# Kernel tuning notes

Measured on AMD Instinct MI355X. Metric: run time of the kernel, lower is better.

Reference implementation:

```python
import jax, jax.numpy as jnp
import numpy as np

K = 3
LAMBDA_AMP = 0.1
N_NODES = 100000
N_EDGES = 1600000
D_FEAT = 50


def _proximal_l21(x, lambda_):
    # rowwise L2,1 shrinkage: scale each row by max(||row||-lambda,0)/||row||
    row_norm = jnp.linalg.norm(x, axis=1)  # [N]
    score = jnp.maximum(row_norm - lambda_, 0.0)
    score = jnp.where(row_norm > 0, score / jnp.where(row_norm > 0, row_norm, 1.0), score)
    return score[:, None] * x


def setup_inputs() -> dict:
    key = jax.random.key(0)
    k1, k2, k3, k4 = jax.random.split(key, 4)
    feat = jax.random.normal(k1, (N_NODES, D_FEAT), dtype=jnp.float32)
    edge_weight = jax.random.uniform(k2, (N_EDGES,), dtype=jnp.float32)
    src = jax.random.randint(k3, (N_EDGES,), 0, N_NODES, dtype=jnp.int32)
    dst = jax.random.randint(k4, (N_EDGES,), 0, N_NODES, dtype=jnp.int32)
    return {"feat": feat, "edge_weight": edge_weight, "src": src, "dst": dst}


def reference(feat, edge_weight, src, dst):
    n = feat.shape[0]
    # add self-loops (add_self_loop=True), self-loop weight = 1
    loop = jnp.arange(n, dtype=src.dtype)
    src_f = jnp.concatenate([src, loop])
    dst_f = jnp.concatenate([dst, loop])
    ew = jnp.concatenate([edge_weight, jnp.ones((n,), dtype=edge_weight.dtype)])

    # norm='both': w_ji = ew / (sqrt(out_deg(j)) * sqrt(in_deg(i))), weighted degrees
    out_deg = jax.ops.segment_sum(ew, src_f, num_segments=n)
    in_deg = jax.ops.segment_sum(ew, dst_f, num_segments=n)
    inv_sqrt_out = jnp.where(out_deg > 0, out_deg, 1.0) ** -0.5 * (out_deg > 0)
    inv_sqrt_in = jnp.where(in_deg > 0, in_deg, 1.0) ** -0.5 * (in_deg > 0)
    w = ew * inv_sqrt_out[src_f] * inv_sqrt_in[dst_f]  # [E+N]

    lam = LAMBDA_AMP
    gamma = 1.0 / (2.0 * (1.0 - lam))
    hh = feat
    x = feat
    for _ in range(K):
        # compute_LX: x - A_norm x  (u_mul_e + sum == SpMM over edges)
        agg = jax.ops.segment_sum(x[src_f] * w[:, None], dst_f, num_segments=n)
        lx = x - agg
        y = x - gamma * 2.0 * (1.0 - lam) * lx
        x = hh + _proximal_l21(y - hh, gamma * lam)
    return x
```

## Files before the change

### kernel.cpp

```cpp
#include <hip/hip_runtime.h>
#include <hip/hip_bf16.h>
#include <hip/hip_fp16.h>

#define D 50
#define PADH 64
#define GLAM 0.05555555555555555f
#define SCAN_B 1024
#define FIXS 8388608.0f
#define INV_FIXS (1.0f / 8388608.0f)
#define WSC 32768.0f
#define INV_WSC (1.0f / 32768.0f)
#define EPB 8192
#define B2T 512
#define BSH 9
#define BMSK 511u
#define BT 512
#define MAXB 256
#define MAXRUN 12288

typedef unsigned long long u64;

__global__ void k_b1p(const int* __restrict__ src, const int* __restrict__ dst,
                      int* __restrict__ mat, const float* __restrict__ feat,
                      __half* __restrict__ xp, int e, int nblk, int nbuk, int n) {
    if ((int)blockIdx.x < nblk) {
        __shared__ unsigned hd[MAXB], hs[MAXB];
        for (int j = threadIdx.x; j < nbuk; j += blockDim.x) { hd[j] = 0; hs[j] = 0; }
        __syncthreads();
        int base = blockIdx.x * EPB;
        int end = base + EPB; if (end > e) end = e;
        for (int i = base + threadIdx.x; i < end; i += blockDim.x) {
            int t = __builtin_nontemporal_load(dst + i);
            int s = __builtin_nontemporal_load(src + i);
            atomicAdd(&hd[t >> BSH], 1u);
            atomicAdd(&hs[s >> BSH], 1u);
        }
        __syncthreads();
        for (int j = threadIdx.x; j < nbuk; j += blockDim.x) {
            mat[j * nblk + blockIdx.x] = (int)hd[j];
            mat[(nbuk + j) * nblk + blockIdx.x] = (int)hs[j];
        }
    } else {
        int i = ((int)blockIdx.x - nblk) * (int)blockDim.x + (int)threadIdx.x;
        if (i < n * PADH) {
            int node = i >> 6, col = i & 63;
            xp[i] = (col < D) ? __float2half_rn(feat[node * D + col]) : __half(0.0f);
        }
    }
}

__global__ void k_scan1(const int* __restrict__ cnt, int* __restrict__ out,
                        int* __restrict__ bsum, int n) {
    __shared__ int s[SCAN_B];
    int i = blockIdx.x * SCAN_B + threadIdx.x;
    int v = (i < n) ? cnt[i] : 0;
    s[threadIdx.x] = v; __syncthreads();
    for (int off = 1; off < SCAN_B; off <<= 1) {
        int t = (threadIdx.x >= (unsigned)off) ? s[threadIdx.x - off] : 0;
        __syncthreads();
        s[threadIdx.x] += t; __syncthreads();
    }
    if (i < n) out[i] = s[threadIdx.x] - v;
    if (threadIdx.x == SCAN_B - 1) bsum[blockIdx.x] = s[threadIdx.x];
}

__global__ void k_scan2(int* __restrict__ bsum, int nb) {
    __shared__ int s[SCAN_B];
    int v = (threadIdx.x < (unsigned)nb) ? bsum[threadIdx.x] : 0;
    s[threadIdx.x] = v; __syncthreads();
    for (int off = 1; off < SCAN_B; off <<= 1) {
        int t = (threadIdx.x >= (unsigned)off) ? s[threadIdx.x - off] : 0;
        __syncthreads();
        s[threadIdx.x] += t; __syncthreads();
    }
    if (threadIdx.x < (unsigned)nb) bsum[threadIdx.x] = s[threadIdx.x] - v;
}

__global__ void k_scan3(int* __restrict__ out, const int* __restrict__ bsum, int n) {
    int i = blockIdx.x * SCAN_B + threadIdx.x;
    if (i < n) out[i] += bsum[blockIdx.x];
}

__global__ void k_b2(const float* __restrict__ ew, const int* __restrict__ src,
                     const int* __restrict__ dst, const int* __restrict__ msc,
                     u64* __restrict__ bind, unsigned* __restrict__ bins,
                     int e, int nblk, int nbuk) {
    __shared__ unsigned cd[MAXB], cs[MAXB];
    __shared__ unsigned ld[MAXB], ls[MAXB];
    __shared__ int gbd[MAXB], gbs[MAXB];
    __shared__ u64 sd[EPB];
    __shared__ unsigned ss[EPB];
    __shared__ unsigned char bdd[EPB], bds[EPB];
    int tid = threadIdx.x;
    for (int j = tid; j < MAXB; j += blockDim.x) { cd[j] = 0; cs[j] = 0; }
    __syncthreads();
    int base = blockIdx.x * EPB;
    int end = base + EPB; if (end > e) end = e;
    int m = end - base;

    for (int i = base + tid; i < end; i += blockDim.x) {
        atomicAdd(&cd[(unsigned)__builtin_nontemporal_load(dst + i) >> BSH], 1u);
        atomicAdd(&cs[(unsigned)__builtin_nontemporal_load(src + i) >> BSH], 1u);
    }
    __syncthreads();

    unsigned vd = 0, vs = 0;
    if (tid < MAXB) { vd = cd[tid]; vs = cs[tid]; ld[tid] = vd; ls[tid] = vs; }
    __syncthreads();
    for (int off = 1; off < MAXB; off <<= 1) {
        unsigned td = 0, ts = 0;
        if (tid < MAXB && tid >= off) { td = ld[tid - off]; ts = ls[tid - off]; }
        __syncthreads();
        if (tid < MAXB) { ld[tid] += td; ls[tid] += ts; }
        __syncthreads();
    }
    if (tid < MAXB) {
        ld[tid] -= vd; ls[tid] -= vs;
        cd[tid] = ld[tid]; cs[tid] = ls[tid];
        if (tid < nbuk) {
            gbd[tid] = msc[tid * nblk + blockIdx.x];
            gbs[tid] = msc[(nbuk + tid) * nblk + blockIdx.x] - e;
        }
    }
    __syncthreads();

    for (int i = base + tid; i < end; i += blockDim.x) {
        float w = __builtin_nontemporal_load(ew + i);
        int s = __builtin_nontemporal_load(src + i);
        int t = __builtin_nontemporal_load(dst + i);
        unsigned wfix = (unsigned)(w * FIXS + 0.5f);
        if (wfix > 0x7FFFFFu) wfix = 0x7FFFFFu;
        unsigned tb = (unsigned)t >> BSH, sb = (unsigned)s >> BSH;
        unsigned pd = atomicAdd(&cd[tb], 1u);
        sd[pd] = ((u64)__float_as_uint(w) << 32)
               | ((unsigned)s << BSH) | (unsigned)(t & BMSK);
        bdd[pd] = (unsigned char)tb;
        unsigned ps = atomicAdd(&cs[sb], 1u);
        ss[ps] = (wfix << BSH) | (unsigned)(s & BMSK);
        bds[ps] = (unsigned char)sb;
    }
    __syncthreads();

    for (int p = tid; p < m; p += blockDim.x) {
        unsigned jd = bdd[p];
        bind[gbd[jd] + (int)(p - ld[jd])] = sd[p];
        unsigned js = bds[p];
        bins[gbs[js] + (int)(p - ls[js])] = ss[p];
    }
}

__global__ void k_srcdeg(const unsigned* __restrict__ bins, const int* __restrict__ msc,
                         float* __restrict__ iso, int n, int nblk, int nbuk, int e) {
    __shared__ unsigned wl[BT];
    wl[threadIdx.x] = 0;
    __syncthreads();
    int b = blockIdx.x;
    int start = msc[(nbuk + b) * nblk] - e;
    int end = (b + 1 < nbuk) ? (msc[(nbuk + b + 1) * nblk] - e) : e;
    for (int i = start + threadIdx.x; i < end; i += blockDim.x) {
        unsigned r = bins[i];
        atomicAdd(&wl[r & BMSK], r >> BSH);
    }
    __syncthreads();
    int node = b * BT + threadIdx.x;
    if (node < n)
        iso[node] = rsqrtf(1.0f + (float)wl[threadIdx.x] * INV_FIXS);
}

__global__ void k_dstfill(const u64* __restrict__ bind, const int* __restrict__ msc,
                          const float* __restrict__ iso, float* __restrict__ isi,
                          int* __restrict__ cnt, int* __restrict__ rowptr,
                          unsigned* __restrict__ pe, int n, int nblk, int nbuk, int e) {
    __shared__ u64 recs[MAXRUN];
    __shared__ unsigned cl[BT], wl[BT], cur[BT];
    __shared__ int sc[BT];
    __shared__ float isL[BT];
    cl[threadIdx.x] = 0; wl[threadIdx.x] = 0;
    __syncthreads();
    int b = blockIdx.x;
    int start = msc[b * nblk];
    int end = (b + 1 < nbuk) ? msc[(b + 1) * nblk] : e;
    int run = end - start;
    bool fast = (run <= MAXRUN);

    if (fast) {
        for (int i = threadIdx.x; i < run; i += blockDim.x) {
            u64 r = bind[start + i];
            recs[i] = r;
            unsigned loc = (unsigned)r & BMSK;
            float w = __uint_as_float((unsigned)(r >> 32));
            unsigned wfix = (unsigned)(w * FIXS + 0.5f);
            if (wfix > 0x7FFFFFu) wfix = 0x7FFFFFu;
            atomicAdd(&cl[loc], 1u);
            atomicAdd(&wl[loc], wfix);
        }
    } else {
        for (int i = start + threadIdx.x; i < end; i += blockDim.x) {
            u64 r = bind[i];
            unsigned loc = (unsigned)r & BMSK;
            float w = __uint_as_float((unsigned)(r >> 32));
            unsigned wfix = (unsigned)(w * FIXS + 0.5f);
            if (wfix > 0x7FFFFFu) wfix = 0x7FFFFFu;
            atomicAdd(&cl[loc], 1u);
            atomicAdd(&wl[loc], wfix);
        }
    }
    __syncthreads();

    int myc = (int)cl[threadIdx.x];
    sc[threadIdx.x] = myc;
    __syncthreads();
    for (int off = 1; off < BT; off <<= 1) {
        int t = (threadIdx.x >= (unsigned)off) ? sc[threadIdx.x - off] : 0;
        __syncthreads();
        sc[threadIdx.x] += t;
        __syncthreads();
    }
    int lrp = start + sc[threadIdx.x] - myc;

    float myisi = rsqrtf(1.0f + (float)wl[threadIdx.x] * INV_FIXS);
    isL[threadIdx.x] = myisi;
    cur[threadIdx.x] = (unsigned)lrp;

    int node = b * BT + threadIdx.x;
    if (node < n) {
        isi[node] = myisi;
        cnt[node] = myc;
        rowptr[node] = lrp;
    }
    __syncthreads();

    if (fast) {
        for (int i = threadIdx.x; i < run; i += blockDim.x) {
            u64 r = recs[i];
            unsigned lo = (unsigned)r;
            unsigned tloc = lo & BMSK;
            unsigned s = lo >> BSH;
            float w = __uint_as_float((unsigned)(r >> 32));
            float wv = w * iso[s] * isL[tloc];
            unsigned wq = (unsigned)(wv * WSC + 0.5f);
            if (wq > 32767u) wq = 32767u;
            unsigned pos = atomicAdd(&cur[tloc], 1u);
            pe[pos] = (s << 15) | wq;
        }
    } else {
        for (int i = start + threadIdx.x; i < end; i += blockDim.x) {
            u64 r = bind[i];
            unsigned lo = (unsigned)r;
            unsigned tloc = lo & BMSK;
            unsigned s = lo >> BSH;
            float w = __uint_as_float((unsigned)(r >> 32));
            float wv = w * iso[s] * isL[tloc];
            unsigned wq = (unsigned)(wv * WSC + 0.5f);
            if (wq > 32767u) wq = 32767u;
            unsigned pos = atomicAdd(&cur[tloc], 1u);
            pe[pos] = (s << 15) | wq;
        }
    }
}

__device__ __forceinline__ void acc_edge(const uint4& u, float w,
                                         float& a0, float& a1, float& a2, float& a3,
                                         float& a4, float& a5, float& a6, float& a7) {
    const __half2* hp = (const __half2*)&u;
    float2 f0 = __half22float2(hp[0]);
    float2 f1 = __half22float2(hp[1]);
    float2 f2 = __half22float2(hp[2]);
    float2 f3 = __half22float2(hp[3]);
    a0 = fmaf(w, f0.x, a0); a1 = fmaf(w, f0.y, a1);
    a2 = fmaf(w, f1.x, a2); a3 = fmaf(w, f1.y, a3);
    a4 = fmaf(w, f2.x, a4); a5 = fmaf(w, f2.y, a5);
    a6 = fmaf(w, f3.x, a6); a7 = fmaf(w, f3.y, a7);
}

__global__ void k_iter(const int* __restrict__ rowptr, const int* __restrict__ cnt,
                       const unsigned* __restrict__ pe, const __half* __restrict__ xin,
                       const __half* __restrict__ xpF, const float* __restrict__ iso,
                       const float* __restrict__ isi, __half* __restrict__ hout,
                       float* __restrict__ fout, int n, int final_iter) {
    int lane = threadIdx.x & 63;
    int c    = lane & 7;
    int waveId = (blockIdx.x * blockDim.x + threadIdx.x) >> 6;
    int node = waveId * 8 + (lane >> 3);
    if (node >= n) return;

    float a0 = 0.f, a1 = 0.f, a2 = 0.f, a3 = 0.f;
    float a4 = 0.f, a5 = 0.f, a6 = 0.f, a7 = 0.f;

    int beg = rowptr[node], m = cnt[node];

    int j = 0;
    for (; j + 4 <= m; j += 4) {
        unsigned p0 = pe[beg + j];
        unsigned p1 = pe[beg + j + 1];
        unsigned p2 = pe[beg + j + 2];
        unsigned p3 = pe[beg + j + 3];
        unsigned s0 = p0 >> 15; float w0 = (float)(p0 & 32767u) * INV_WSC;
        unsigned s1 = p1 >> 15; float w1 = (float)(p1 & 32767u) * INV_WSC;
        unsigned s2 = p2 >> 15; float w2 = (float)(p2 & 32767u) * INV_WSC;
        unsigned s3 = p3 >> 15; float w3 = (float)(p3 & 32767u) * INV_WSC;
        uint4 u0 = *(const uint4*)(xin + ((size_t)s0 << 6) + (c << 3));
        uint4 u1 = *(const uint4*)(xin + ((size_t)s1 << 6) + (c << 3));
        uint4 u2 = *(const uint4*)(xin + ((size_t)s2 << 6) + (c << 3));
        uint4 u3 = *(const uint4*)(xin + ((size_t)s3 << 6) + (c << 3));
        acc_edge(u0, w0, a0, a1, a2, a3, a4, a5, a6, a7);
        acc_edge(u1, w1, a0, a1, a2, a3, a4, a5, a6, a7);
        acc_edge(u2, w2, a0, a1, a2, a3, a4, a5, a6, a7);
        acc_edge(u3, w3, a0, a1, a2, a3, a4, a5, a6, a7);
    }
    for (; j < m; ++j) {
        unsigned p0 = pe[beg + j];
        unsigned s0 = p0 >> 15;
        float    w0 = (float)(p0 & 32767u) * INV_WSC;
        uint4 u0 = *(const uint4*)(xin + ((size_t)s0 << 6) + (c << 3));
        acc_edge(u0, w0, a0, a1, a2, a3, a4, a5, a6, a7);
    }

    float selfw = iso[node] * isi[node];
    {
        uint4 u = *(const uint4*)(xin + ((size_t)node << 6) + (c << 3));
        acc_edge(u, selfw, a0, a1, a2, a3, a4, a5, a6, a7);
    }

    float f[8];
    {
        uint4 u = *(const uint4*)(xpF + ((size_t)node << 6) + (c << 3));
        const __half2* hp = (const __half2*)&u;
        float2 f0 = __half22float2(hp[0]);
        float2 f1 = __half22float2(hp[1]);
        float2 f2 = __half22float2(hp[2]);
        float2 f3 = __half22float2(hp[3]);
        f[0] = f0.x; f[1] = f0.y; f[2] = f1.x; f[3] = f1.y;
        f[4] = f2.x; f[5] = f2.y; f[6] = f3.x; f[7] = f3.y;
    }

    float d0 = a0 - f[0], d1 = a1 - f[1], d2 = a2 - f[2], d3 = a3 - f[3];
    float d4 = a4 - f[4], d5 = a5 - f[5], d6 = a6 - f[6], d7 = a7 - f[7];

    float ssum = d0*d0 + d1*d1 + d2*d2 + d3*d3 + d4*d4 + d5*d5 + d6*d6 + d7*d7;
    ssum += __shfl_xor(ssum, 1, 64);
    ssum += __shfl_xor(ssum, 2, 64);
    ssum += __shfl_xor(ssum, 4, 64);
    float norm = sqrtf(ssum);
    float sc = (norm > 0.0f) ? fmaxf(norm - GLAM, 0.0f) / norm : 0.0f;

    float o0 = f[0] + sc * d0, o1 = f[1] + sc * d1;
    float o2 = f[2] + sc * d2, o3 = f[3] + sc * d3;
    float o4 = f[4] + sc * d4, o5 = f[5] + sc * d5;
    float o6 = f[6] + sc * d6, o7 = f[7] + sc * d7;
    if (!final_iter) {
        __half2 h0 = __float22half2_rn(make_float2(o0, o1));
        __half2 h1 = __float22half2_rn(make_float2(o2, o3));
        __half2 h2 = __float22half2_rn(make_float2(o4, o5));
        __half2 h3 = __float22half2_rn(make_float2(o6, o7));
        uint4 u;
        u.x = *(unsigned*)&h0; u.y = *(unsigned*)&h1;
        u.z = *(unsigned*)&h2; u.w = *(unsigned*)&h3;
        *(uint4*)(hout + ((size_t)node << 6) + (c << 3)) = u;
    } else {
        float o[8] = {o0, o1, o2, o3, o4, o5, o6, o7};
        int fb = c << 3;
        #pragma unroll
        for (int k = 0; k < 4; ++k) {
            int ff = fb + (k << 1);
            if (ff + 1 < D) {
                float2 v; v.x = o[k * 2]; v.y = o[k * 2 + 1];
                *(float2*)(fout + (size_t)node * D + ff) = v;
            }
        }
    }
}

extern "C" void kernel_launch(void* const* d_in, const int* in_sizes, int n_in,
                              void* d_out, int out_size, void* d_ws, size_t ws_size,
                              hipStream_t stream) {
    const float* feat = (const float*)d_in[0];
    const float* ew   = (const float*)d_in[1];
    const int* src = (const int*)d_in[2];
    const int* dst = (const int*)d_in[3];

    const int nd = in_sizes[0];
    const int n  = nd / D;
    const int e  = in_sizes[1];
    const int np = n * PADH;

    const int nbuk = (n + BT - 1) / BT;
    const int nblk = (e + EPB - 1) / EPB;
    const int nm   = 2 * nbuk * nblk;

    __half*   xpF    = (__half*)d_ws;
    __half*   xpA    = xpF + np;
    __half*   xpB    = xpA + np;
    u64*      bind   = (u64*)(xpB + np);
    unsigned* pe     = (unsigned*)(bind + e);
    unsigned* bins   = pe + e;
    int*      mat    = (int*)(bins + e);
    int*      msc    = mat + nm;
    float*    isi    = (float*)(msc + nm);
    float*    iso    = isi + n;
    int*      cnt    = (int*)(iso + n);
    int*      rowptr = cnt + n;
    int*      bsum   = rowptr + n;
    float*    out    = (float*)d_out;

    const int B = 256;
    const int gP  = (np + B2T - 1) / B2T;
    const int NBm = (nm + SCAN_B - 1) / SCAN_B;

    k_b1p<<<nblk + gP, B2T, 0, stream>>>(src, dst, mat, feat, xpF, e, nblk, nbuk, n);
    k_scan1<<<NBm, SCAN_B, 0, stream>>>(mat, msc, bsum, nm);
    k_scan2<<<1, SCAN_B, 0, stream>>>(bsum, NBm);
    k_scan3<<<NBm, SCAN_B, 0, stream>>>(msc, bsum, nm);
    k_b2<<<nblk, B2T, 0, stream>>>(ew, src, dst, msc, bind, bins, e, nblk, nbuk);
    k_srcdeg<<<nbuk, BT, 0, stream>>>(bins, msc, iso, n, nblk, nbuk, e);
    k_dstfill<<<nbuk, BT, 0, stream>>>(bind, msc, iso, isi, cnt, rowptr, pe, n, nblk, nbuk, e);

    const int nodesPerBlock = (B / 64) * 8;
    const int iterGrid = (n + nodesPerBlock - 1) / nodesPerBlock;

    k_iter<<<iterGrid, B, 0, stream>>>(rowptr, cnt, pe, xpF, xpF, iso, isi, xpA, out, n, 0);
    k_iter<<<iterGrid, B, 0, stream>>>(rowptr, cnt, pe, xpA, xpF, iso, isi, xpB, out, n, 0);
    k_iter<<<iterGrid, B, 0, stream>>>(rowptr, cnt, pe, xpB, xpF, iso, isi, xpA, out, n, 1);
}
```

Measured before the change: 254.5 us.

## Compute source degrees via global atomics and degree-sort nodes for SpMM

Drops the source-side bucketing pass (per-block source histogram, source bin scatter and the k_srcdeg kernel). Source weighted degrees are now accumulated directly with global atomicAdd into a per-node array, followed by a small rsqrt kernel. It also builds a degree histogram and a counting-sort permutation so each k_iter wave handles nodes of similar in-degree, which reduces divergence inside a wave, and it marks pe loads as nontemporal. The cost is 1.6M scattered global atomics, one extra indirection per node in the iteration kernels, and less locality in output writes.

After: 338.5 us. 1.33x slower.

```diff
diff --git a/kernel.cpp b/kernel.cpp
--- a/kernel.cpp
+++ b/kernel.cpp
@@ -17,35 +17,36 @@
 #define BT 512
 #define MAXB 256
 #define MAXRUN 12288
+#define DEGB 64
 
 typedef unsigned long long u64;
 
 __global__ void k_b1p(const int* __restrict__ src, const int* __restrict__ dst,
                       int* __restrict__ mat, const float* __restrict__ feat,
-                      __half* __restrict__ xp, int e, int nblk, int nbuk, int n) {
+                      __half* __restrict__ xp, unsigned* __restrict__ degS,
+                      unsigned* __restrict__ dcur, unsigned* __restrict__ dhist,
+                      int e, int nblk, int nbuk, int n) {
     if ((int)blockIdx.x < nblk) {
-        __shared__ unsigned hd[MAXB], hs[MAXB];
-        for (int j = threadIdx.x; j < nbuk; j += blockDim.x) { hd[j] = 0; hs[j] = 0; }
+        __shared__ unsigned hd[MAXB];
+        for (int j = threadIdx.x; j < nbuk; j += blockDim.x) hd[j] = 0;
         __syncthreads();
         int base = blockIdx.x * EPB;
         int end = base + EPB; if (end > e) end = e;
         for (int i = base + threadIdx.x; i < end; i += blockDim.x) {
             int t = __builtin_nontemporal_load(dst + i);
-            int s = __builtin_nontemporal_load(src + i);
             atomicAdd(&hd[t >> BSH], 1u);
-            atomicAdd(&hs[s >> BSH], 1u);
-        }
-        __syncthreads();
-        for (int j = threadIdx.x; j < nbuk; j += blockDim.x) {
+        }
+        __syncthreads();
+        for (int j = threadIdx.x; j < nbuk; j += blockDim.x)
             mat[j * nblk + blockIdx.x] = (int)hd[j];
-            mat[(nbuk + j) * nblk + blockIdx.x] = (int)hs[j];
-        }
     } else {
         int i = ((int)blockIdx.x - nblk) * (int)blockDim.x + (int)threadIdx.x;
         if (i < n * PADH) {
             int node = i >> 6, col = i & 63;
             xp[i] = (col < D) ? __float2half_rn(feat[node * D + col]) : __half(0.0f);
         }
+        if (i < n) degS[i] = 0u;
+        if (i < DEGB) { dcur[i] = 0u; dhist[i] = 0u; }
     }
 }
 
@@ -81,46 +82,41 @@
     if (i < n) out[i] += bsum[blockIdx.x];
 }
 
-__global__ void k_b2(const float* __restrict__ ew, const int* __restrict__ src,
+__global__ __launch_bounds__(B2T, 4) void k_b2(
+                     const float* __restrict__ ew, const int* __restrict__ src,
                      const int* __restrict__ dst, const int* __restrict__ msc,
-                     u64* __restrict__ bind, unsigned* __restrict__ bins,
+                     u64* __restrict__ bind, unsigned* __restrict__ degS,
                      int e, int nblk, int nbuk) {
-    __shared__ unsigned cd[MAXB], cs[MAXB];
-    __shared__ unsigned ld[MAXB], ls[MAXB];
-    __shared__ int gbd[MAXB], gbs[MAXB];
+    __shared__ unsigned cd[MAXB];
+    __shared__ unsigned ld[MAXB];
+    __shared__ int gbd[MAXB];
     __shared__ u64 sd[EPB];
-    __shared__ unsigned ss[EPB];
-    __shared__ unsigned char bdd[EPB], bds[EPB];
+    __shared__ unsigned char bdd[EPB];
     int tid = threadIdx.x;
-    for (int j = tid; j < MAXB; j += blockDim.x) { cd[j] = 0; cs[j] = 0; }
+    for (int j = tid; j < MAXB; j += blockDim.x) cd[j] = 0;
     __syncthreads();
     int base = blockIdx.x * EPB;
     int end = base + EPB; if (end > e) end = e;
     int m = end - base;
 
-    for (int i = base + tid; i < end; i += blockDim.x) {
+    for (int i = base + tid; i < end; i += blockDim.x)
         atomicAdd(&cd[(unsigned)__builtin_nontemporal_load(dst + i) >> BSH], 1u);
-        atomicAdd(&cs[(unsigned)__builtin_nontemporal_load(src + i) >> BSH], 1u);
-    }
-    __syncthreads();
-
-    unsigned vd = 0, vs = 0;
-    if (tid < MAXB) { vd = cd[tid]; vs = cs[tid]; ld[tid] = vd; ls[tid] = vs; }
+    __syncthreads();
+
+    unsigned vd = 0;
+    if (tid < MAXB) { vd = cd[tid]; ld[tid] = vd; }
     __syncthreads();
     for (int off = 1; off < MAXB; off <<= 1) {
-        unsigned td = 0, ts = 0;
-        if (tid < MAXB && tid >= off) { td = ld[tid - off]; ts = ls[tid - off]; }
-        __syncthreads();
-        if (tid < MAXB) { ld[tid] += td; ls[tid] += ts; }
+        unsigned td = 0;
+        if (tid < MAXB && tid >= off) td = ld[tid - off];
+        __syncthreads();
+        if (tid < MAXB) ld[tid] += td;
         __syncthreads();
     }
     if (tid < MAXB) {
-        ld[tid] -= vd; ls[tid] -= vs;
-        cd[tid] = ld[tid]; cs[tid] = ls[tid];
-        if (tid < nbuk) {
-            gbd[tid] = msc[tid * nblk + blockIdx.x];
-            gbs[tid] = msc[(nbuk + tid) * nblk + blockIdx.x] - e;
-        }
+        ld[tid] -= vd;
+        cd[tid] = ld[tid];
+        if (tid < nbuk) gbd[tid] = msc[tid * nblk + blockIdx.x];
     }
     __syncthreads();
 
@@ -130,52 +126,38 @@
         int t = __builtin_nontemporal_load(dst + i);
         unsigned wfix = (unsigned)(w * FIXS + 0.5f);
         if (wfix > 0x7FFFFFu) wfix = 0x7FFFFFu;
-        unsigned tb = (unsigned)t >> BSH, sb = (unsigned)s >> BSH;
+        atomicAdd(&degS[s], wfix);
+        unsigned tb = (unsigned)t >> BSH;
         unsigned pd = atomicAdd(&cd[tb], 1u);
         sd[pd] = ((u64)__float_as_uint(w) << 32)
                | ((unsigned)s << BSH) | (unsigned)(t & BMSK);
         bdd[pd] = (unsigned char)tb;
-        unsigned ps = atomicAdd(&cs[sb], 1u);
-        ss[ps] = (wfix << BSH) | (unsigned)(s & BMSK);
-        bds[ps] = (unsigned char)sb;
     }
     __syncthreads();
 
     for (int p = tid; p < m; p += blockDim.x) {
         unsigned jd = bdd[p];
         bind[gbd[jd] + (int)(p - ld[jd])] = sd[p];
-        unsigned js = bds[p];
-        bins[gbs[js] + (int)(p - ls[js])] = ss[p];
-    }
-}
-
-__global__ void k_srcdeg(const unsigned* __restrict__ bins, const int* __restrict__ msc,
-                         float* __restrict__ iso, int n, int nblk, int nbuk, int e) {
-    __shared__ unsigned wl[BT];
-    wl[threadIdx.x] = 0;
-    __syncthreads();
-    int b = blockIdx.x;
-    int start = msc[(nbuk + b) * nblk] - e;
-    int end = (b + 1 < nbuk) ? (msc[(nbuk + b + 1) * nblk] - e) : e;
-    for (int i = start + threadIdx.x; i < end; i += blockDim.x) {
-        unsigned r = bins[i];
-        atomicAdd(&wl[r & BMSK], r >> BSH);
-    }
-    __syncthreads();
-    int node = b * BT + threadIdx.x;
-    if (node < n)
-        iso[node] = rsqrtf(1.0f + (float)wl[threadIdx.x] * INV_FIXS);
+    }
+}
+
+__global__ void k_iso(const unsigned* __restrict__ degS, float* __restrict__ iso, int n) {
+    int i = blockIdx.x * blockDim.x + threadIdx.x;
+    if (i < n) iso[i] = rsqrtf(1.0f + (float)degS[i] * INV_FIXS);
 }
 
 __global__ void k_dstfill(const u64* __restrict__ bind, const int* __restrict__ msc,
                           const float* __restrict__ iso, float* __restrict__ isi,
                           int* __restrict__ cnt, int* __restrict__ rowptr,
-                          unsigned* __restrict__ pe, int n, int nblk, int nbuk, int e) {
+                          unsigned* __restrict__ pe, unsigned* __restrict__ dhist,
+                          int n, int nblk, int nbuk, int e) {
     __shared__ u64 recs[MAXRUN];
     __shared__ unsigned cl[BT], wl[BT], cur[BT];
     __shared__ int sc[BT];
     __shared__ float isL[BT];
+    __shared__ unsigned dh[DEGB];
     cl[threadIdx.x] = 0; wl[threadIdx.x] = 0;
+    if (threadIdx.x < DEGB) dh[threadIdx.x] = 0;
     __syncthreads();
     int b = blockIdx.x;
     int start = msc[b * nblk];
@@ -227,8 +209,12 @@
         isi[node] = myisi;
         cnt[node] = myc;
         rowptr[node] = lrp;
-    }
-    __syncthreads();
+        int dg = myc < (DEGB - 1) ? myc : (DEGB - 1);
+        atomicAdd(&dh[dg], 1u);
+    }
+    __syncthreads();
+    if (threadIdx.x < DEGB && dh[threadIdx.x])
+        atomicAdd(&dhist[threadIdx.x], dh[threadIdx.x]);
 
     if (fast) {
         for (int i = threadIdx.x; i < run; i += blockDim.x) {
@@ -259,6 +245,30 @@
     }
 }
 
+__global__ void k_dscat(const int* __restrict__ cnt, const unsigned* __restrict__ dhist,
+                        unsigned* __restrict__ dcur, int* __restrict__ perm, int n) {
+    __shared__ unsigned lh[DEGB], lb[DEGB], gb[DEGB], hco[DEGB];
+    int tid = threadIdx.x;
+    if (tid < DEGB) { lh[tid] = 0; hco[tid] = dhist[tid]; }
+    __syncthreads();
+    int i = blockIdx.x * blockDim.x + tid;
+    int d = 0; unsigned lrank = 0;
+    if (i < n) {
+        int c = cnt[i];
+        d = c < (DEGB - 1) ? c : (DEGB - 1);
+        lrank = atomicAdd(&lh[d], 1u);
+    }
+    __syncthreads();
+    if (tid < DEGB) {
+        unsigned s = 0;
+        for (int j = 0; j < tid; ++j) s += hco[j];
+        gb[tid] = s;
+        lb[tid] = lh[tid] ? atomicAdd(&dcur[tid], lh[tid]) : 0u;
+    }
+    __syncthreads();
+    if (i < n) perm[gb[d] + lb[d] + lrank] = i;
+}
+
 __device__ __forceinline__ void acc_edge(const uint4& u, float w,
                                          float& a0, float& a1, float& a2, float& a3,
                                          float& a4, float& a5, float& a6, float& a7) {
@@ -274,15 +284,17 @@
 }
 
 __global__ void k_iter(const int* __restrict__ rowptr, const int* __restrict__ cnt,
-                       const unsigned* __restrict__ pe, const __half* __restrict__ xin,
+                       const unsigned* __restrict__ pe, const int* __restrict__ perm,
+                       const __half* __restrict__ xin,
                        const __half* __restrict__ xpF, const float* __restrict__ iso,
                        const float* __restrict__ isi, __half* __restrict__ hout,
                        float* __restrict__ fout, int n, int final_iter) {
     int lane = threadIdx.x & 63;
     int c    = lane & 7;
     int waveId = (blockIdx.x * blockDim.x + threadIdx.x) >> 6;
-    int node = waveId * 8 + (lane >> 3);
-    if (node >= n) return;
+    int slot = waveId * 8 + (lane >> 3);
+    if (slot >= n) return;
+    int node = perm[slot];
 
     float a0 = 0.f, a1 = 0.f, a2 = 0.f, a3 = 0.f;
     float a4 = 0.f, a5 = 0.f, a6 = 0.f, a7 = 0.f;
@@ -291,10 +303,10 @@
 
     int j = 0;
     for (; j + 4 <= m; j += 4) {
-        unsigned p0 = pe[beg + j];
-        unsigned p1 = pe[beg + j + 1];
-        unsigned p2 = pe[beg + j + 2];
-        unsigned p3 = pe[beg + j + 3];
+        unsigned p0 = __builtin_nontemporal_load(pe + beg + j);
+        unsigned p1 = __builtin_nontemporal_load(pe + beg + j + 1);
+        unsigned p2 = __builtin_nontemporal_load(pe + beg + j + 2);
+        unsigned p3 = __builtin_nontemporal_load(pe + beg + j + 3);
         unsigned s0 = p0 >> 15; float w0 = (float)(p0 & 32767u) * INV_WSC;
         unsigned s1 = p1 >> 15; float w1 = (float)(p1 & 32767u) * INV_WSC;
         unsigned s2 = p2 >> 15; float w2 = (float)(p2 & 32767u) * INV_WSC;
@@ -309,7 +321,7 @@
         acc_edge(u3, w3, a0, a1, a2, a3, a4, a5, a6, a7);
     }
     for (; j < m; ++j) {
-        unsigned p0 = pe[beg + j];
+        unsigned p0 = __builtin_nontemporal_load(pe + beg + j);
         unsigned s0 = p0 >> 15;
         float    w0 = (float)(p0 & 32767u) * INV_WSC;
         uint4 u0 = *(const uint4*)(xin + ((size_t)s0 << 6) + (c << 3));
@@ -386,39 +398,45 @@
 
     const int nbuk = (n + BT - 1) / BT;
     const int nblk = (e + EPB - 1) / EPB;
-    const int nm   = 2 * nbuk * nblk;
+    const int nm   = nbuk * nblk;
 
     __half*   xpF    = (__half*)d_ws;
     __half*   xpA    = xpF + np;
     __half*   xpB    = xpA + np;
     u64*      bind   = (u64*)(xpB + np);
     unsigned* pe     = (unsigned*)(bind + e);
-    unsigned* bins   = pe + e;
-    int*      mat    = (int*)(bins + e);
+    int*      mat    = (int*)(pe + e);
     int*      msc    = mat + nm;
     float*    isi    = (float*)(msc + nm);
     float*    iso    = isi + n;
     int*      cnt    = (int*)(iso + n);
     int*      rowptr = cnt + n;
-    int*      bsum   = rowptr + n;
+    unsigned* degS   = (unsigned*)(rowptr + n);
+    int*      perm   = (int*)(degS + n);
+    unsigned* dhist  = (unsigned*)(perm + n);
+    unsigned* dcur   = dhist + DEGB;
+    int*      bsum   = (int*)(dcur + DEGB);
     float*    out    = (float*)d_out;
 
     const int B = 256;
     const int gP  = (np + B2T - 1) / B2T;
     const int NBm = (nm + SCAN_B - 1) / SCAN_B;
 
-    k_b1p<<<nblk + gP, B2T, 0, stream>>>(src, dst, mat, feat, xpF, e, nblk, nbuk, n);
+    k_b1p<<<nblk + gP, B2T, 0, stream>>>(src, dst, mat, feat, xpF, degS, dcur, dhist,
+                                         e, nblk, nbuk, n);
     k_scan1<<<NBm, SCAN_B, 0, stream>>>(mat, msc, bsum, nm);
     k_scan2<<<1, SCAN_B, 0, stream>>>(bsum, NBm);
     k_scan3<<<NBm, SCAN_B, 0, stream>>>(msc, bsum, nm);
-    k_b2<<<nblk, B2T, 0, stream>>>(ew, src, dst, msc, bind, bins, e, nblk, nbuk);
-    k_srcdeg<<<nbuk, BT, 0, stream>>>(bins, msc, iso, n, nblk, nbuk, e);
-    k_dstfill<<<nbuk, BT, 0, stream>>>(bind, msc, iso, isi, cnt, rowptr, pe, n, nblk, nbuk, e);
+    k_b2<<<nblk, B2T, 0, stream>>>(ew, src, dst, msc, bind, degS, e, nblk, nbuk);
+    k_iso<<<(n + 255) / 256, 256, 0, stream>>>(degS, iso, n);
+    k_dstfill<<<nbuk, BT, 0, stream>>>(bind, msc, iso, isi, cnt, rowptr, pe, dhist,
+                                       n, nblk, nbuk, e);
+    k_dscat<<<(n + 255) / 256, 256, 0, stream>>>(cnt, dhist, dcur, perm, n);
 
     const int nodesPerBlock = (B / 64) * 8;
     const int iterGrid = (n + nodesPerBlock - 1) / nodesPerBlock;
 
-    k_iter<<<iterGrid, B, 0, stream>>>(rowptr, cnt, pe, xpF, xpF, iso, isi, xpA, out, n, 0);
-    k_iter<<<iterGrid, B, 0, stream>>>(rowptr, cnt, pe, xpA, xpF, iso, isi, xpB, out, n, 0);
-    k_iter<<<iterGrid, B, 0, stream>>>(rowptr, cnt, pe, xpB, xpF, iso, isi, xpA, out, n, 1);
-}
+    k_iter<<<iterGrid, B, 0, stream>>>(rowptr, cnt, pe, perm, xpF, xpF, iso, isi, xpA, out, n, 0);
+    k_iter<<<iterGrid, B, 0, stream>>>(rowptr, cnt, pe, perm, xpA, xpF, iso, isi, xpB, out, n, 0);
+    k_iter<<<iterGrid, B, 0, stream>>>(rowptr, cnt, pe, perm, xpB, xpF, iso, isi, xpA, out, n, 1);
+}
```

## Sort nodes by in-degree for balanced SpMM waves; halve edges per block

Applied to the files above, without the earlier changes.

Builds a degree histogram in the dst-fill kernel and adds a scatter kernel that writes a node permutation grouped by in-degree. The SpMM iteration kernels then process nodes in that order, so the 8 nodes sharing a wave have similar edge counts and lanes wait less on each other. It also halves the edges per binning block (more blocks, more bucket-matrix entries to scan) and adds launch bounds to the binning kernel. The costs are an extra kernel, an extra indirection per node, and output writes scattered across node order rather than contiguous.

After: 272.2 us. +7.0%, slower.

```diff
diff --git a/kernel.cpp b/kernel.cpp
--- a/kernel.cpp
+++ b/kernel.cpp
@@ -10,19 +10,22 @@
 #define INV_FIXS (1.0f / 8388608.0f)
 #define WSC 32768.0f
 #define INV_WSC (1.0f / 32768.0f)
-#define EPB 8192
+#define EPB 4096
 #define B2T 512
 #define BSH 9
 #define BMSK 511u
 #define BT 512
 #define MAXB 256
 #define MAXRUN 12288
+#define DEGB 64
 
 typedef unsigned long long u64;
 
 __global__ void k_b1p(const int* __restrict__ src, const int* __restrict__ dst,
                       int* __restrict__ mat, const float* __restrict__ feat,
-                      __half* __restrict__ xp, int e, int nblk, int nbuk, int n) {
+                      __half* __restrict__ xp, unsigned* __restrict__ dcur,
+                      unsigned* __restrict__ dhist,
+                      int e, int nblk, int nbuk, int n) {
     if ((int)blockIdx.x < nblk) {
         __shared__ unsigned hd[MAXB], hs[MAXB];
         for (int j = threadIdx.x; j < nbuk; j += blockDim.x) { hd[j] = 0; hs[j] = 0; }
@@ -46,6 +49,7 @@
             int node = i >> 6, col = i & 63;
             xp[i] = (col < D) ? __float2half_rn(feat[node * D + col]) : __half(0.0f);
         }
+        if (i < DEGB) { dcur[i] = 0u; dhist[i] = 0u; }
     }
 }
 
@@ -81,7 +85,8 @@
     if (i < n) out[i] += bsum[blockIdx.x];
 }
 
-__global__ void k_b2(const float* __restrict__ ew, const int* __restrict__ src,
+__global__ __launch_bounds__(B2T, 4) void k_b2(
+                     const float* __restrict__ ew, const int* __restrict__ src,
                      const int* __restrict__ dst, const int* __restrict__ msc,
                      u64* __restrict__ bind, unsigned* __restrict__ bins,
                      int e, int nblk, int nbuk) {
@@ -170,12 +175,15 @@
 __global__ void k_dstfill(const u64* __restrict__ bind, const int* __restrict__ msc,
                           const float* __restrict__ iso, float* __restrict__ isi,
                           int* __restrict__ cnt, int* __restrict__ rowptr,
-                          unsigned* __restrict__ pe, int n, int nblk, int nbuk, int e) {
+                          unsigned* __restrict__ pe, unsigned* __restrict__ dhist,
+                          int n, int nblk, int nbuk, int e) {
     __shared__ u64 recs[MAXRUN];
     __shared__ unsigned cl[BT], wl[BT], cur[BT];
     __shared__ int sc[BT];
     __shared__ float isL[BT];
+    __shared__ unsigned dh[DEGB];
     cl[threadIdx.x] = 0; wl[threadIdx.x] = 0;
+    if (threadIdx.x < DEGB) dh[threadIdx.x] = 0;
     __syncthreads();
     int b = blockIdx.x;
     int start = msc[b * nblk];
@@ -227,8 +235,12 @@
         isi[node] = myisi;
         cnt[node] = myc;
         rowptr[node] = lrp;
-    }
-    __syncthreads();
+        int dg = myc < (DEGB - 1) ? myc : (DEGB - 1);
+        atomicAdd(&dh[dg], 1u);
+    }
+    __syncthreads();
+    if (threadIdx.x < DEGB && dh[threadIdx.x])
+        atomicAdd(&dhist[threadIdx.x], dh[threadIdx.x]);
 
     if (fast) {
         for (int i = threadIdx.x; i < run; i += blockDim.x) {
@@ -259,6 +271,30 @@
     }
 }
 
+__global__ void k_dscat(const int* __restrict__ cnt, const unsigned* __restrict__ dhist,
+                        unsigned* __restrict__ dcur, int* __restrict__ perm, int n) {
+    __shared__ unsigned lh[DEGB], lb[DEGB], gb[DEGB], hco[DEGB];
+    int tid = threadIdx.x;
+    if (tid < DEGB) { lh[tid] = 0; hco[tid] = dhist[tid]; }
+    __syncthreads();
+    int i = blockIdx.x * blockDim.x + tid;
+    int d = 0; unsigned lrank = 0;
+    if (i < n) {
+        int c = cnt[i];
+        d = c < (DEGB - 1) ? c : (DEGB - 1);
+        lrank = atomicAdd(&lh[d], 1u);
+    }
+    __syncthreads();
+    if (tid < DEGB) {
+        unsigned s = 0;
+        for (int j = 0; j < tid; ++j) s += hco[j];
+        gb[tid] = s;
+        lb[tid] = lh[tid] ? atomicAdd(&dcur[tid], lh[tid]) : 0u;
+    }
+    __syncthreads();
+    if (i < n) perm[gb[d] + lb[d] + lrank] = i;
+}
+
 __device__ __forceinline__ void acc_edge(const uint4& u, float w,
                                          float& a0, float& a1, float& a2, float& a3,
                                          float& a4, float& a5, float& a6, float& a7) {
@@ -274,15 +310,17 @@
 }
 
 __global__ void k_iter(const int* __restrict__ rowptr, const int* __restrict__ cnt,
-                       const unsigned* __restrict__ pe, const __half* __restrict__ xin,
+                       const unsigned* __restrict__ pe, const int* __restrict__ perm,
+                       const __half* __restrict__ xin,
                        const __half* __restrict__ xpF, const float* __restrict__ iso,
                        const float* __restrict__ isi, __half* __restrict__ hout,
                        float* __restrict__ fout, int n, int final_iter) {
     int lane = threadIdx.x & 63;
     int c    = lane & 7;
     int waveId = (blockIdx.x * blockDim.x + threadIdx.x) >> 6;
-    int node = waveId * 8 + (lane >> 3);
-    if (node >= n) return;
+    int slot = waveId * 8 + (lane >> 3);
+    if (slot >= n) return;
+    int node = perm[slot];
 
     float a0 = 0.f, a1 = 0.f, a2 = 0.f, a3 = 0.f;
     float a4 = 0.f, a5 = 0.f, a6 = 0.f, a7 = 0.f;
@@ -400,25 +438,31 @@
     float*    iso    = isi + n;
     int*      cnt    = (int*)(iso + n);
     int*      rowptr = cnt + n;
-    int*      bsum   = rowptr + n;
+    int*      perm   = rowptr + n;
+    unsigned* dhist  = (unsigned*)(perm + n);
+    unsigned* dcur   = dhist + DEGB;
+    int*      bsum   = (int*)(dcur + DEGB);
     float*    out    = (float*)d_out;
 
     const int B = 256;
     const int gP  = (np + B2T - 1) / B2T;
     const int NBm = (nm + SCAN_B - 1) / SCAN_B;
 
-    k_b1p<<<nblk + gP, B2T, 0, stream>>>(src, dst, mat, feat, xpF, e, nblk, nbuk, n);
+    k_b1p<<<nblk + gP, B2T, 0, stream>>>(src, dst, mat, feat, xpF, dcur, dhist,
+                                         e, nblk, nbuk, n);
     k_scan1<<<NBm, SCAN_B, 0, stream>>>(mat, msc, bsum, nm);
     k_scan2<<<1, SCAN_B, 0, stream>>>(bsum, NBm);
     k_scan3<<<NBm, SCAN_B, 0, stream>>>(msc, bsum, nm);
     k_b2<<<nblk, B2T, 0, stream>>>(ew, src, dst, msc, bind, bins, e, nblk, nbuk);
     k_srcdeg<<<nbuk, BT, 0, stream>>>(bins, msc, iso, n, nblk, nbuk, e);
-    k_dstfill<<<nbuk, BT, 0, stream>>>(bind, msc, iso, isi, cnt, rowptr, pe, n, nblk, nbuk, e);
+    k_dstfill<<<nbuk, BT, 0, stream>>>(bind, msc, iso, isi, cnt, rowptr, pe, dhist,
+                                       n, nblk, nbuk, e);
+    k_dscat<<<(n + 255) / 256, 256, 0, stream>>>(cnt, dhist, dcur, perm, n);
 
     const int nodesPerBlock = (B / 64) * 8;
     const int iterGrid = (n + nodesPerBlock - 1) / nodesPerBlock;
 
-    k_iter<<<iterGrid, B, 0, stream>>>(rowptr, cnt, pe, xpF, xpF, iso, isi, xpA, out, n, 0);
-    k_iter<<<iterGrid, B, 0, stream>>>(rowptr, cnt, pe, xpA, xpF, iso, isi, xpB, out, n, 0);
-    k_iter<<<iterGrid, B, 0, stream>>>(rowptr, cnt, pe, xpB, xpF, iso, isi, xpA, out, n, 1);
-}
+    k_iter<<<iterGrid, B, 0, stream>>>(rowptr, cnt, pe, perm, xpF, xpF, iso, isi, xpA, out, n, 0);
+    k_iter<<<iterGrid, B, 0, stream>>>(rowptr, cnt, pe, perm, xpA, xpF, iso, isi, xpB, out, n, 0);
+    k_iter<<<iterGrid, B, 0, stream>>>(rowptr, cnt, pe, perm, xpB, xpF, iso, isi, xpA, out, n, 1);
+}
```

## Replace per-block count matrix scan with global bucket atomics and direct scatter

Applied to the files above, without the earlier changes.

The bucket sort preprocessing no longer builds a per-block-by-bucket count matrix and scans it in three kernels. Instead, global per-bucket totals are accumulated with atomics and scanned by a single small kernel. Each placement block then reserves its output ranges with one global atomic per bucket and writes records straight to global memory, skipping the shared-memory staging. The SpMM gather loop also gains an 8-way unrolled path to keep more loads in flight. The trade-off is that the order of edges within a bucket becomes nondeterministic and the global writes are less coalesced.

After: 276.5 us. 1.09x slower.

```diff
diff --git a/kernel.cpp b/kernel.cpp
--- a/kernel.cpp
+++ b/kernel.cpp
@@ -5,11 +5,11 @@
 #define D 50
 #define PADH 64
 #define GLAM 0.05555555555555555f
-#define SCAN_B 1024
 #define FIXS 8388608.0f
 #define INV_FIXS (1.0f / 8388608.0f)
 #define WSC 32768.0f
 #define INV_WSC (1.0f / 32768.0f)
+#define ECB 16384
 #define EPB 8192
 #define B2T 512
 #define BSH 9
@@ -17,18 +17,20 @@
 #define BT 512
 #define MAXB 256
 #define MAXRUN 12288
+#define GSTR 16
 
 typedef unsigned long long u64;
 
-__global__ void k_b1p(const int* __restrict__ src, const int* __restrict__ dst,
-                      int* __restrict__ mat, const float* __restrict__ feat,
-                      __half* __restrict__ xp, int e, int nblk, int nbuk, int n) {
-    if ((int)blockIdx.x < nblk) {
+__global__ void k_count(const int* __restrict__ src, const int* __restrict__ dst,
+                        unsigned* __restrict__ totD, unsigned* __restrict__ totS,
+                        const float* __restrict__ feat, __half* __restrict__ xp,
+                        int e, int ncb, int nbuk, int n) {
+    if ((int)blockIdx.x < ncb) {
         __shared__ unsigned hd[MAXB], hs[MAXB];
         for (int j = threadIdx.x; j < nbuk; j += blockDim.x) { hd[j] = 0; hs[j] = 0; }
         __syncthreads();
-        int base = blockIdx.x * EPB;
-        int end = base + EPB; if (end > e) end = e;
+        int base = blockIdx.x * ECB;
+        int end = base + ECB; if (end > e) end = e;
         for (int i = base + threadIdx.x; i < end; i += blockDim.x) {
             int t = __builtin_nontemporal_load(dst + i);
             int s = __builtin_nontemporal_load(src + i);
@@ -37,11 +39,11 @@
         }
         __syncthreads();
         for (int j = threadIdx.x; j < nbuk; j += blockDim.x) {
-            mat[j * nblk + blockIdx.x] = (int)hd[j];
-            mat[(nbuk + j) * nblk + blockIdx.x] = (int)hs[j];
+            if (hd[j]) atomicAdd(&totD[j], hd[j]);
+            if (hs[j]) atomicAdd(&totS[j], hs[j]);
         }
     } else {
-        int i = ((int)blockIdx.x - nblk) * (int)blockDim.x + (int)threadIdx.x;
+        int i = ((int)blockIdx.x - ncb) * (int)blockDim.x + (int)threadIdx.x;
         if (i < n * PADH) {
             int node = i >> 6, col = i & 63;
             xp[i] = (col < D) ? __float2half_rn(feat[node * D + col]) : __half(0.0f);
@@ -49,54 +51,43 @@
     }
 }
 
-__global__ void k_scan1(const int* __restrict__ cnt, int* __restrict__ out,
-                        int* __restrict__ bsum, int n) {
-    __shared__ int s[SCAN_B];
-    int i = blockIdx.x * SCAN_B + threadIdx.x;
-    int v = (i < n) ? cnt[i] : 0;
-    s[threadIdx.x] = v; __syncthreads();
-    for (int off = 1; off < SCAN_B; off <<= 1) {
-        int t = (threadIdx.x >= (unsigned)off) ? s[threadIdx.x - off] : 0;
+__global__ void k_scanS(const unsigned* __restrict__ totD, const unsigned* __restrict__ totS,
+                        unsigned* __restrict__ gcur, int* __restrict__ basesD,
+                        int* __restrict__ basesS, int nbuk, int e) {
+    __shared__ unsigned s[B2T];
+    int tid = threadIdx.x;
+    unsigned v = 0;
+    if (tid < nbuk) v = totD[tid];
+    else if (tid < 2 * nbuk) v = totS[tid - nbuk];
+    s[tid] = v; __syncthreads();
+    for (int off = 1; off < B2T; off <<= 1) {
+        unsigned t = (tid >= off) ? s[tid - off] : 0;
         __syncthreads();
-        s[threadIdx.x] += t; __syncthreads();
-    }
-    if (i < n) out[i] = s[threadIdx.x] - v;
-    if (threadIdx.x == SCAN_B - 1) bsum[blockIdx.x] = s[threadIdx.x];
-}
-
-__global__ void k_scan2(int* __restrict__ bsum, int nb) {
-    __shared__ int s[SCAN_B];
-    int v = (threadIdx.x < (unsigned)nb) ? bsum[threadIdx.x] : 0;
-    s[threadIdx.x] = v; __syncthreads();
-    for (int off = 1; off < SCAN_B; off <<= 1) {
-        int t = (threadIdx.x >= (unsigned)off) ? s[threadIdx.x - off] : 0;
-        __syncthreads();
-        s[threadIdx.x] += t; __syncthreads();
-    }
-    if (threadIdx.x < (unsigned)nb) bsum[threadIdx.x] = s[threadIdx.x] - v;
-}
-
-__global__ void k_scan3(int* __restrict__ out, const int* __restrict__ bsum, int n) {
-    int i = blockIdx.x * SCAN_B + threadIdx.x;
-    if (i < n) out[i] += bsum[blockIdx.x];
-}
-
-__global__ void k_b2(const float* __restrict__ ew, const int* __restrict__ src,
-                     const int* __restrict__ dst, const int* __restrict__ msc,
+        s[tid] += t; __syncthreads();
+    }
+    unsigned excl = s[tid] - v;
+    if (tid < nbuk) {
+        gcur[tid * GSTR] = excl;
+        basesD[tid] = (int)excl;
+    } else if (tid < 2 * nbuk) {
+        unsigned b = excl - (unsigned)e;
+        gcur[(MAXB + (tid - nbuk)) * GSTR] = b;
+        basesS[tid - nbuk] = (int)b;
+    }
+    if (tid == 0) { basesD[nbuk] = e; basesS[nbuk] = e; }
+}
+
+__global__ __launch_bounds__(B2T) void k_place(
+                     const float* __restrict__ ew, const int* __restrict__ src,
+                     const int* __restrict__ dst, unsigned* __restrict__ gcur,
                      u64* __restrict__ bind, unsigned* __restrict__ bins,
-                     int e, int nblk, int nbuk) {
+                     int e, int nbuk) {
     __shared__ unsigned cd[MAXB], cs[MAXB];
-    __shared__ unsigned ld[MAXB], ls[MAXB];
-    __shared__ int gbd[MAXB], gbs[MAXB];
-    __shared__ u64 sd[EPB];
-    __shared__ unsigned ss[EPB];
-    __shared__ unsigned char bdd[EPB], bds[EPB];
     int tid = threadIdx.x;
     for (int j = tid; j < MAXB; j += blockDim.x) { cd[j] = 0; cs[j] = 0; }
     __syncthreads();
     int base = blockIdx.x * EPB;
     int end = base + EPB; if (end > e) end = e;
-    int m = end - base;
 
     for (int i = base + tid; i < end; i += blockDim.x) {
         atomicAdd(&cd[(unsigned)__builtin_nontemporal_load(dst + i) >> BSH], 1u);
@@ -104,23 +95,11 @@
     }
     __syncthreads();
 
-    unsigned vd = 0, vs = 0;
-    if (tid < MAXB) { vd = cd[tid]; vs = cs[tid]; ld[tid] = vd; ls[tid] = vs; }
-    __syncthreads();
-    for (int off = 1; off < MAXB; off <<= 1) {
-        unsigned td = 0, ts = 0;
-        if (tid < MAXB && tid >= off) { td = ld[tid - off]; ts = ls[tid - off]; }
-        __syncthreads();
-        if (tid < MAXB) { ld[tid] += td; ls[tid] += ts; }
-        __syncthreads();
-    }
-    if (tid < MAXB) {
-        ld[tid] -= vd; ls[tid] -= vs;
-        cd[tid] = ld[tid]; cs[tid] = ls[tid];
-        if (tid < nbuk) {
-            gbd[tid] = msc[tid * nblk + blockIdx.x];
-            gbs[tid] = msc[(nbuk + tid) * nblk + blockIdx.x] - e;
-        }
+    if (tid < nbuk) {
+        unsigned h = cd[tid];
+        cd[tid] = h ? atomicAdd(&gcur[tid * GSTR], h) : 0u;
+        h = cs[tid];
+        cs[tid] = h ? atomicAdd(&gcur[(MAXB + tid) * GSTR], h) : 0u;
     }
     __syncthreads();
 
@@ -132,31 +111,21 @@
         if (wfix > 0x7FFFFFu) wfix = 0x7FFFFFu;
         unsigned tb = (unsigned)t >> BSH, sb = (unsigned)s >> BSH;
         unsigned pd = atomicAdd(&cd[tb], 1u);
-        sd[pd] = ((u64)__float_as_uint(w) << 32)
-               | ((unsigned)s << BSH) | (unsigned)(t & BMSK);
-        bdd[pd] = (unsigned char)tb;
+        bind[pd] = ((u64)__float_as_uint(w) << 32)
+                 | ((unsigned)s << BSH) | (unsigned)(t & BMSK);
         unsigned ps = atomicAdd(&cs[sb], 1u);
-        ss[ps] = (wfix << BSH) | (unsigned)(s & BMSK);
-        bds[ps] = (unsigned char)sb;
-    }
-    __syncthreads();
-
-    for (int p = tid; p < m; p += blockDim.x) {
-        unsigned jd = bdd[p];
-        bind[gbd[jd] + (int)(p - ld[jd])] = sd[p];
-        unsigned js = bds[p];
-        bins[gbs[js] + (int)(p - ls[js])] = ss[p];
-    }
-}
-
-__global__ void k_srcdeg(const unsigned* __restrict__ bins, const int* __restrict__ msc,
-                         float* __restrict__ iso, int n, int nblk, int nbuk, int e) {
+        bins[ps] = (wfix << BSH) | (unsigned)(s & BMSK);
+    }
+}
+
+__global__ void k_srcdeg(const unsigned* __restrict__ bins, const int* __restrict__ basesS,
+                         float* __restrict__ iso, int n) {
     __shared__ unsigned wl[BT];
     wl[threadIdx.x] = 0;
     __syncthreads();
     int b = blockIdx.x;
-    int start = msc[(nbuk + b) * nblk] - e;
-    int end = (b + 1 < nbuk) ? (msc[(nbuk + b + 1) * nblk] - e) : e;
+    int start = basesS[b];
+    int end = basesS[b + 1];
     for (int i = start + threadIdx.x; i < end; i += blockDim.x) {
         unsigned r = bins[i];
         atomicAdd(&wl[r & BMSK], r >> BSH);
@@ -167,10 +136,10 @@
         iso[node] = rsqrtf(1.0f + (float)wl[threadIdx.x] * INV_FIXS);
 }
 
-__global__ void k_dstfill(const u64* __restrict__ bind, const int* __restrict__ msc,
+__global__ void k_dstfill(const u64* __restrict__ bind, const int* __restrict__ basesD,
                           const float* __restrict__ iso, float* __restrict__ isi,
                           int* __restrict__ cnt, int* __restrict__ rowptr,
-                          unsigned* __restrict__ pe, int n, int nblk, int nbuk, int e) {
+                          unsigned* __restrict__ pe, int n, int e) {
     __shared__ u64 recs[MAXRUN];
     __shared__ unsigned cl[BT], wl[BT], cur[BT];
     __shared__ int sc[BT];
@@ -178,8 +147,8 @@
     cl[threadIdx.x] = 0; wl[threadIdx.x] = 0;
     __syncthreads();
     int b = blockIdx.x;
-    int start = msc[b * nblk];
-    int end = (b + 1 < nbuk) ? msc[(b + 1) * nblk] : e;
+    int start = basesD[b];
+    int end = basesD[b + 1];
     int run = end - start;
     bool fast = (run <= MAXRUN);
 
@@ -290,6 +259,40 @@
     int beg = rowptr[node], m = cnt[node];
 
     int j = 0;
+    for (; j + 8 <= m; j += 8) {
+        unsigned p0 = pe[beg + j];
+        unsigned p1 = pe[beg + j + 1];
+        unsigned p2 = pe[beg + j + 2];
+        unsigned p3 = pe[beg + j + 3];
+        unsigned p4 = pe[beg + j + 4];
+        unsigned p5 = pe[beg + j + 5];
+        unsigned p6 = pe[beg + j + 6];
+        unsigned p7 = pe[beg + j + 7];
+        unsigned s0 = p0 >> 15; float w0 = (float)(p0 & 32767u) * INV_WSC;
+        unsigned s1 = p1 >> 15; float w1 = (float)(p1 & 32767u) * INV_WSC;
+        unsigned s2 = p2 >> 15; float w2 = (float)(p2 & 32767u) * INV_WSC;
+        unsigned s3 = p3 >> 15; float w3 = (float)(p3 & 32767u) * INV_WSC;
+        unsigned s4 = p4 >> 15; float w4 = (float)(p4 & 32767u) * INV_WSC;
+        unsigned s5 = p5 >> 15; float w5 = (float)(p5 & 32767u) * INV_WSC;
+        unsigned s6 = p6 >> 15; float w6 = (float)(p6 & 32767u) * INV_WSC;
+        unsigned s7 = p7 >> 15; float w7 = (float)(p7 & 32767u) * INV_WSC;
+        uint4 u0 = *(const uint4*)(xin + ((size_t)s0 << 6) + (c << 3));
+        uint4 u1 = *(const uint4*)(xin + ((size_t)s1 << 6) + (c << 3));
+        uint4 u2 = *(const uint4*)(xin + ((size_t)s2 << 6) + (c << 3));
+        uint4 u3 = *(const uint4*)(xin + ((size_t)s3 << 6) + (c << 3));
+        uint4 u4 = *(const uint4*)(xin + ((size_t)s4 << 6) + (c << 3));
+        uint4 u5 = *(const uint4*)(xin + ((size_t)s5 << 6) + (c << 3));
+        uint4 u6 = *(const uint4*)(xin + ((size_t)s6 << 6) + (c << 3));
+        uint4 u7 = *(const uint4*)(xin + ((size_t)s7 << 6) + (c << 3));
+        acc_edge(u0, w0, a0, a1, a2, a3, a4, a5, a6, a7);
+        acc_edge(u1, w1, a0, a1, a2, a3, a4, a5, a6, a7);
+        acc_edge(u2, w2, a0, a1, a2, a3, a4, a5, a6, a7);
+        acc_edge(u3, w3, a0, a1, a2, a3, a4, a5, a6, a7);
+        acc_edge(u4, w4, a0, a1, a2, a3, a4, a5, a6, a7);
+        acc_edge(u5, w5, a0, a1, a2, a3, a4, a5, a6, a7);
+        acc_edge(u6, w6, a0, a1, a2, a3, a4, a5, a6, a7);
+        acc_edge(u7, w7, a0, a1, a2, a3, a4, a5, a6, a7);
+    }
     for (; j + 4 <= m; j += 4) {
         unsigned p0 = pe[beg + j];
         unsigned p1 = pe[beg + j + 1];
@@ -385,8 +388,8 @@
     const int np = n * PADH;
 
     const int nbuk = (n + BT - 1) / BT;
-    const int nblk = (e + EPB - 1) / EPB;
-    const int nm   = 2 * nbuk * nblk;
+    const int ncb  = (e + ECB - 1) / ECB;
+    const int nplc = (e + EPB - 1) / EPB;
 
     __half*   xpF    = (__half*)d_ws;
     __half*   xpA    = xpF + np;
@@ -394,26 +397,26 @@
     u64*      bind   = (u64*)(xpB + np);
     unsigned* pe     = (unsigned*)(bind + e);
     unsigned* bins   = pe + e;
-    int*      mat    = (int*)(bins + e);
-    int*      msc    = mat + nm;
-    float*    isi    = (float*)(msc + nm);
+    unsigned* totD   = bins + e;
+    unsigned* totS   = totD + MAXB;
+    unsigned* gcur   = totS + MAXB;
+    int*      basesD = (int*)(gcur + 2 * MAXB * GSTR);
+    int*      basesS = basesD + MAXB + 1;
+    float*    isi    = (float*)(basesS + MAXB + 1);
     float*    iso    = isi + n;
     int*      cnt    = (int*)(iso + n);
     int*      rowptr = cnt + n;
-    int*      bsum   = rowptr + n;
     float*    out    = (float*)d_out;
 
     const int B = 256;
-    const int gP  = (np + B2T - 1) / B2T;
-    const int NBm = (nm + SCAN_B - 1) / SCAN_B;
-
-    k_b1p<<<nblk + gP, B2T, 0, stream>>>(src, dst, mat, feat, xpF, e, nblk, nbuk, n);
-    k_scan1<<<NBm, SCAN_B, 0, stream>>>(mat, msc, bsum, nm);
-    k_scan2<<<1, SCAN_B, 0, stream>>>(bsum, NBm);
-    k_scan3<<<NBm, SCAN_B, 0, stream>>>(msc, bsum, nm);
-    k_b2<<<nblk, B2T, 0, stream>>>(ew, src, dst, msc, bind, bins, e, nblk, nbuk);
-    k_srcdeg<<<nbuk, BT, 0, stream>>>(bins, msc, iso, n, nblk, nbuk, e);
-    k_dstfill<<<nbuk, BT, 0, stream>>>(bind, msc, iso, isi, cnt, rowptr, pe, n, nblk, nbuk, e);
+    const int gP = (np + B2T - 1) / B2T;
+
+    hipMemsetAsync(totD, 0, 2 * MAXB * sizeof(unsigned), stream);
+    k_count<<<ncb + gP, B2T, 0, stream>>>(src, dst, totD, totS, feat, xpF, e, ncb, nbuk, n);
+    k_scanS<<<1, B2T, 0, stream>>>(totD, totS, gcur, basesD, basesS, nbuk, e);
+    k_place<<<nplc, B2T, 0, stream>>>(ew, src, dst, gcur, bind, bins, e, nbuk);
+    k_srcdeg<<<nbuk, BT, 0, stream>>>(bins, basesS, iso, n);
+    k_dstfill<<<nbuk, BT, 0, stream>>>(bind, basesD, iso, isi, cnt, rowptr, pe, n, e);
 
     const int nodesPerBlock = (B / 64) * 8;
     const int iterGrid = (n + nodesPerBlock - 1) / nodesPerBlock;
```
